# Optimization experiments

Hardware: AMD Instinct MI355X
Metric: run time of the kernel (lower is better)

The kernel has to match this reference:

```python
import jax, jax.numpy as jnp
import numpy as np

# config constants (init_kwargs)
WC, WS = 0.5, 0.5            # boundary cosine / structural weights (hybrid mode)
TARGET_BPP = 6.0             # target_bytes_per_patch
GAIN = 1.0                   # target_patch_gain
THRESH = 0.5                 # boundary_threshold; mask = p >= THRESH
EPS = 1e-6

_POP6 = jnp.array([bin(i).count('1') for i in range(64)], dtype=jnp.int32)

def _pop6(x):
    return _POP6[jnp.clip(x, 0, 63)]

def _logit(p):
    p = jnp.clip(p, EPS, 1.0 - EPS)
    return jnp.log(p) - jnp.log1p(-p)

def _next(x):  # shift-left by one, zero-padded at end (matches torch q_next pattern)
    return jnp.concatenate([x[1:], jnp.zeros((1,), x.dtype)])

def _hist(vals, mask, bins):
    idx = jnp.where(mask, vals, bins)  # invalid -> out of range, dropped
    return jnp.zeros((bins,), jnp.int32).at[idx].add(1, mode='drop')


def setup_inputs() -> dict:
    key = jax.random.key(0)
    ks = jax.random.split(key, 6)
    B, S = 4, 1048576
    return {
        'boundary_logprobs': jax.random.normal(ks[0], (B, S), jnp.float32),
        'states': jax.random.randint(ks[1], (B, S), 0, 4096, jnp.int32),
        'q_class': jax.random.randint(ks[2], (B, S), 0, 64, jnp.int32),
        'family': jax.random.randint(ks[3], (B, S), 0, 4, jnp.int32),
        'micro_ref': jax.random.randint(ks[4], (B, S), 0, 64, jnp.int32),
        'valid_mask': jax.random.randint(ks[5], (B, S), 0, 2, jnp.int32).astype(bool),
    }


def reference(boundary_logprobs, states, q_class, family, micro_ref, valid_mask):
    B, S = valid_mask.shape
    v = valid_mask.reshape(-1)
    st = states.reshape(-1).astype(jnp.int32)
    q = q_class.reshape(-1).astype(jnp.int32)
    fam = family.reshape(-1).astype(jnp.int32)
    mic = micro_ref.reshape(-1).astype(jnp.int32)

    # --- structural boundary probs ---
    omega12 = st & 0xFFF
    c6 = ((omega12 >> 6) ^ omega12) & 63          # chirality6
    d_chi = jnp.clip(_pop6(c6 ^ _next(c6)).astype(jnp.float32) / 6.0, 0.0, 1.0)
    d_q = _pop6((q & 63) ^ (_next(q) & 63)).astype(jnp.float32) / 6.0
    fx = (fam & 3) ^ (_next(fam) & 3)
    d_fam = (((fx & 1) != 0).astype(jnp.float32) + ((fx & 2) != 0).astype(jnp.float32)) / 2.0
    score = jnp.clip(0.5 * d_chi + 0.35 * d_q + 0.15 * d_fam, EPS, 1.0)
    structural = jnp.where(v, score, 0.0)

    # --- combine with cosine probs (hybrid mode) ---
    cosine = jnp.exp(jnp.minimum(boundary_logprobs.reshape(-1), 0.0))
    combined = (WC * cosine + WS * structural) / max(WC + WS, 1e-6)

    # --- target bytes-per-patch rate adjustment ---
    vf = v.astype(jnp.float32)
    vc = jnp.maximum(jnp.sum(vf), 1.0)
    cur = jnp.clip(jnp.sum(combined * vf) / vc, 1e-4, 1.0 - 1e-4)
    tgt = max(1e-4, min(1.0 - 1e-4, 1.0 / TARGET_BPP))
    shift = _logit(jnp.asarray(tgt, jnp.float32)) - _logit(cur)
    combined = jax.nn.sigmoid(_logit(combined) + GAIN * shift)
    combined = jnp.clip(combined, EPS, 1.0 - EPS)
    combined_logprobs = jnp.log(combined)
    bmask = combined_logprobs >= jnp.log(jnp.asarray(THRESH, jnp.float32))

    # --- histograms over effective (valid) positions ---
    shell = _pop6(c6)
    q_hist64 = _hist(q, v, 64)
    family_hist4 = _hist(fam, v, 4)
    micro_hist64 = _hist(mic, v, 64)
    shell_hist7 = _hist(shell, v, 7)
    wt_q = _pop6(q & 63)
    q_weight_hist7 = _hist(wt_q, v, 7)
    bits = ((q & 63)[:, None] >> jnp.arange(6)) & 1            # [n, 6]
    bit_excitation6 = jnp.sum(bits * v[:, None].astype(jnp.int32), axis=0)

    # --- patch lengths (vectorized run-length over valid bytes) ---
    bv = bmask & v
    pos = jnp.cumsum(v.astype(jnp.int32))                      # 1-indexed valid position
    bpos = jnp.where(bv, pos, 0)
    prev = jax.lax.cummax(jnp.concatenate([jnp.zeros((1,), jnp.int32), bpos[:-1]]))
    lengths = jnp.where(bv, pos - prev, 0)                     # dense run lengths at boundaries
    total_valid = pos[-1]
    trailing = total_valid - jax.lax.cummax(bpos)[-1]          # open trailing run
    patch_count = jnp.sum(bv).astype(jnp.int32) + (trailing > 0).astype(jnp.int32)

    return (combined_logprobs.reshape(B, S), bmask.reshape(B, S), structural.reshape(B, S),
            q_hist64, family_hist4, micro_hist64, shell_hist7, q_weight_hist7,
            bit_excitation6, lengths, trailing, patch_count)
```

## Files before the change

### kernel.cpp

```cpp
#include <hip/hip_runtime.h>

#define TPB 256
#define EPT 8
#define CHUNK (TPB * EPT)
#define P2T 1024
#define NSLICE 64

typedef unsigned long long ull;

__device__ __forceinline__ ull shfl_down_u64(ull x, int off) {
    unsigned lo = (unsigned)x, hi = (unsigned)(x >> 32);
    lo = __shfl_down(lo, off, 64);
    hi = __shfl_down(hi, off, 64);
    return ((ull)hi << 32) | lo;
}

__global__ __launch_bounds__(TPB, 8) void k_pass1(
    const float* __restrict__ blp, const int* __restrict__ st,
    const int* __restrict__ q, const int* __restrict__ fam,
    const int* __restrict__ mic, const int* __restrict__ vm,
    float* __restrict__ out_structural,
    int* __restrict__ blocksum_v, double* __restrict__ blocksum_c,
    int* __restrict__ ghist, int n)
{
    __shared__ int lh2[2048];
    __shared__ int slhs[11];
    __shared__ int swv[4];
    __shared__ float swc[4];

    const int tid = threadIdx.x, lane = tid & 63, wave = tid >> 6;
    const long i0 = (long)blockIdx.x * CHUNK + (long)tid * EPT;
    const bool fast = ((long)(blockIdx.x + 1) * CHUNK <= n);

    int stv[9], qv[9], fv[9], micv[8], vmv[8];
    float bpv[8];
    if (fast) {
        const int4 sa = *(const int4*)(st + i0),  sb = *(const int4*)(st + i0 + 4);
        const int4 qa = *(const int4*)(q + i0),   qb = *(const int4*)(q + i0 + 4);
        const int4 fa = *(const int4*)(fam + i0), fb = *(const int4*)(fam + i0 + 4);
        const int4 ma = *(const int4*)(mic + i0), mb = *(const int4*)(mic + i0 + 4);
        const int4 va = *(const int4*)(vm + i0),  vb = *(const int4*)(vm + i0 + 4);
        const float4 ba = *(const float4*)(blp + i0), bb = *(const float4*)(blp + i0 + 4);
        int nst = __shfl_down(sa.x, 1, 64);
        int nq  = __shfl_down(qa.x, 1, 64);
        int nf  = __shfl_down(fa.x, 1, 64);
        if (lane == 63) {
            const long j = i0 + 8;
            nst = (j < n) ? st[j]  : 0;
            nq  = (j < n) ? q[j]   : 0;
            nf  = (j < n) ? fam[j] : 0;
        }
        stv[0]=sa.x; stv[1]=sa.y; stv[2]=sa.z; stv[3]=sa.w; stv[4]=sb.x; stv[5]=sb.y; stv[6]=sb.z; stv[7]=sb.w; stv[8]=nst;
        qv[0]=qa.x;  qv[1]=qa.y;  qv[2]=qa.z;  qv[3]=qa.w;  qv[4]=qb.x;  qv[5]=qb.y;  qv[6]=qb.z;  qv[7]=qb.w;  qv[8]=nq;
        fv[0]=fa.x;  fv[1]=fa.y;  fv[2]=fa.z;  fv[3]=fa.w;  fv[4]=fb.x;  fv[5]=fb.y;  fv[6]=fb.z;  fv[7]=fb.w;  fv[8]=nf;
        micv[0]=ma.x; micv[1]=ma.y; micv[2]=ma.z; micv[3]=ma.w; micv[4]=mb.x; micv[5]=mb.y; micv[6]=mb.z; micv[7]=mb.w;
        vmv[0]=va.x; vmv[1]=va.y; vmv[2]=va.z; vmv[3]=va.w; vmv[4]=vb.x; vmv[5]=vb.y; vmv[6]=vb.z; vmv[7]=vb.w;
        bpv[0]=ba.x; bpv[1]=ba.y; bpv[2]=ba.z; bpv[3]=ba.w; bpv[4]=bb.x; bpv[5]=bb.y; bpv[6]=bb.z; bpv[7]=bb.w;
    } else {
        #pragma unroll
        for (int e = 0; e < 8; ++e) {
            long ii = i0 + e;
            bool r = ii < n;
            stv[e] = r ? st[ii] : 0;  qv[e] = r ? q[ii] : 0;  fv[e] = r ? fam[ii] : 0;
            micv[e] = r ? mic[ii] : 0; vmv[e] = r ? vm[ii] : 0; bpv[e] = r ? blp[ii] : 0.f;
        }
        stv[8] = (i0 + 8 < n) ? st[i0 + 8] : 0;
        qv[8]  = (i0 + 8 < n) ? q[i0 + 8] : 0;
        fv[8]  = (i0 + 8 < n) ? fam[i0 + 8] : 0;
    }

    {
        int4 z4; z4.x = 0; z4.y = 0; z4.z = 0; z4.w = 0;
        *(int4*)&lh2[tid * 8] = z4;
        *(int4*)&lh2[tid * 8 + 4] = z4;
    }
    if (tid < 11) slhs[tid] = 0;
    __syncthreads();

    const int qrow = ((wave << 2) | (lane & 3)) << 6;
    int sv = 0;
    float scf = 0.0f;
    ull accF = 0, accS0 = 0, accS1 = 0;
    float structural[8];
    #pragma unroll
    for (int e = 0; e < 8; ++e) {
        int sti = stv[e], qi = qv[e], fi = fv[e], mi = micv[e];
        int v = (vmv[e] != 0);
        int om  = sti & 0xFFF;      int c6  = ((om  >> 6) ^ om ) & 63;
        int omn = stv[e+1] & 0xFFF; int c6n = ((omn >> 6) ^ omn) & 63;
        float d_chi = (float)__popc(c6 ^ c6n) * (1.0f / 6.0f);
        float d_q   = (float)__popc((qi & 63) ^ (qv[e+1] & 63)) * (1.0f / 6.0f);
        int fx = (fi & 3) ^ (fv[e+1] & 3);
        float d_fam = (float)((fx & 1) + ((fx >> 1) & 1)) * 0.5f;
        float score = 0.5f * d_chi + 0.35f * d_q + 0.15f * d_fam;
        score = fminf(fmaxf(score, 1e-6f), 1.0f);
        structural[e] = v ? score : 0.0f;
        float cosine = expf(fminf(bpv[e], 0.0f));
        float combined = 0.5f * (cosine + structural[e]);
        if (v) {
            sv += 1;
            scf += combined;
            atomicAdd(&lh2[qrow + (qi & 63)], 1);
            atomicAdd(&lh2[1024 + qrow + (mi & 63)], 1);
            accF += 1ULL << ((fi & 3) * 16);
            int sh = __popc(c6);
            ull ts = 1ULL << ((sh & 3) * 16);
            if (sh < 4) accS0 += ts; else accS1 += ts;
        }
    }

    if (fast) {
        float4 o;
        o.x=structural[0]; o.y=structural[1]; o.z=structural[2]; o.w=structural[3];
        *(float4*)(out_structural + i0) = o;
        o.x=structural[4]; o.y=structural[5]; o.z=structural[6]; o.w=structural[7];
        *(float4*)(out_structural + i0 + 4) = o;
    } else {
        #pragma unroll
        for (int e = 0; e < 8; ++e)
            if (i0 + e < n) out_structural[i0 + e] = structural[e];
    }

    #pragma unroll
    for (int off = 32; off > 0; off >>= 1) {
        sv  += __shfl_down(sv, off, 64);
        scf += __shfl_down(scf, off, 64);
        accF  += shfl_down_u64(accF, off);
        accS0 += shfl_down_u64(accS0, off);
        accS1 += shfl_down_u64(accS1, off);
    }
    if (lane == 0) {
        swv[wave] = sv; swc[wave] = scf;
        #pragma unroll
        for (int b2 = 0; b2 < 4; ++b2) atomicAdd(&slhs[b2],     (int)((accF  >> (16*b2)) & 0xFFFF));
        #pragma unroll
        for (int b2 = 0; b2 < 4; ++b2) atomicAdd(&slhs[4 + b2], (int)((accS0 >> (16*b2)) & 0xFFFF));
        #pragma unroll
        for (int b2 = 0; b2 < 3; ++b2) atomicAdd(&slhs[8 + b2], (int)((accS1 >> (16*b2)) & 0xFFFF));
    }
    __syncthreads();
    if (tid == 0) {
        blocksum_v[blockIdx.x] = swv[0] + swv[1] + swv[2] + swv[3];
        blocksum_c[blockIdx.x] = (double)swc[0] + (double)swc[1] + (double)swc[2] + (double)swc[3];
    }
    int* gh = ghist + (blockIdx.x & (NSLICE - 1)) * 152;
    for (int t2 = tid; t2 < 139; t2 += TPB) {
        int val;
        if (t2 < 64) {
            val = 0;
            #pragma unroll
            for (int r = 0; r < 16; ++r) val += lh2[(r << 6) + t2];
        } else if (t2 < 68) {
            val = slhs[t2 - 64];
        } else if (t2 < 132) {
            int b2 = t2 - 68;
            val = 0;
            #pragma unroll
            for (int r = 0; r < 16; ++r) val += lh2[1024 + (r << 6) + b2];
        } else {
            val = slhs[4 + (t2 - 132)];
        }
        if (val) atomicAdd(&gh[t2], val);
    }
}

__global__ __launch_bounds__(TPB, 8) void k_pass3(
    const float* __restrict__ strc, const float* __restrict__ blp,
    const int* __restrict__ bsv, const double* __restrict__ bsc,
    const int* __restrict__ ghist,
    float* __restrict__ out_logp, float* __restrict__ out_bmask,
    float* __restrict__ out_len, int* __restrict__ chunk_cnt,
    int* __restrict__ chunk_last, ull* __restrict__ chunk_first,
    int* __restrict__ totalv_p, float* __restrict__ out_hist, int n)
{
    __shared__ int swt[4], swm[4], scnt[4];
    __shared__ ull sfirst[4];
    __shared__ int sB[4], sT[4];
    __shared__ double sC[4];
    __shared__ int qh[64];
    const int tid = threadIdx.x, lane = tid & 63, wave = tid >> 6;
    const long i0 = (long)blockIdx.x * CHUNK + (long)tid * EPT;
    const bool fast = ((long)(blockIdx.x + 1) * CHUNK <= n);
    const int nb = (int)gridDim.x;

    float sv8[8], bp8[8];
    if (fast) {
        const float4 s0 = *(const float4*)(strc + i0), s1 = *(const float4*)(strc + i0 + 4);
        const float4 p0 = *(const float4*)(blp + i0),  p1 = *(const float4*)(blp + i0 + 4);
        sv8[0]=s0.x; sv8[1]=s0.y; sv8[2]=s0.z; sv8[3]=s0.w; sv8[4]=s1.x; sv8[5]=s1.y; sv8[6]=s1.z; sv8[7]=s1.w;
        bp8[0]=p0.x; bp8[1]=p0.y; bp8[2]=p0.z; bp8[3]=p0.w; bp8[4]=p1.x; bp8[5]=p1.y; bp8[6]=p1.z; bp8[7]=p1.w;
    } else {
        #pragma unroll
        for (int e = 0; e < 8; ++e) {
            long ii = i0 + e;
            bool r = ii < n;
            sv8[e] = r ? strc[ii] : 0.0f;
            bp8[e] = r ? blp[ii] : 0.0f;
        }
    }

    int bsum = 0, tsum = 0;
    double csum = 0.0;
    for (int c = tid; c < nb; c += TPB) {
        int vv = bsv[c];
        tsum += vv;
        if (c < (int)blockIdx.x) bsum += vv;
        csum += bsc[c];
    }
    #pragma unroll
    for (int off = 32; off > 0; off >>= 1) {
        bsum += __shfl_down(bsum, off, 64);
        tsum += __shfl_down(tsum, off, 64);
        csum += __shfl_down(csum, off, 64);
    }
    if (lane == 0) { sB[wave] = bsum; sT[wave] = tsum; sC[wave] = csum; }
    __syncthreads();
    const int wb0     = sB[0] + sB[1] + sB[2] + sB[3];
    const int total_v = sT[0] + sT[1] + sT[2] + sT[3];
    const double dtot = sC[0] + sC[1] + sC[2] + sC[3];
    float shift;
    {
        double vc = (double)(total_v > 1 ? total_v : 1);
        float cur = (float)(dtot / vc);
        cur = fminf(fmaxf(cur, 1e-4f), 0.9999f);
        float p = fminf(fmaxf(cur, 1e-6f), 0.999999f);
        float lc = logf(p) - log1pf(-p);
        float tgt = (float)(1.0 / 6.0);
        float lt = logf(tgt) - log1pf(-tgt);
        shift = lt - lc;
    }

    unsigned mv = 0, mb = 0;
    float lp[8], bmf[8], lenv[8];
    #pragma unroll
    for (int e = 0; e < 8; ++e) {
        float s = sv8[e];
        int v = (s > 0.0f);
        float cosine = expf(fminf(bp8[e], 0.0f));
        float comb = 0.5f * (cosine + s);
        float p = fminf(fmaxf(comb, 1e-6f), 0.999999f);
        float z = logf(p) - log1pf(-p) + shift;
        float sgm = 1.0f / (1.0f + expf(-z));
        sgm = fminf(fmaxf(sgm, 1e-6f), 0.999999f);
        float clp = logf(sgm);
        lp[e] = clp;
        int bm = (clp >= -0.69314718f) ? 1 : 0;
        bmf[e] = (float)bm;
        mv |= (unsigned)v << e;
        if (bm & v) mb |= 1u << e;
        lenv[e] = 0.0f;
    }
    if (fast) {
        float4 o;
        o.x=lp[0]; o.y=lp[1]; o.z=lp[2]; o.w=lp[3];     *(float4*)(out_logp + i0) = o;
        o.x=lp[4]; o.y=lp[5]; o.z=lp[6]; o.w=lp[7];     *(float4*)(out_logp + i0 + 4) = o;
        o.x=bmf[0]; o.y=bmf[1]; o.z=bmf[2]; o.w=bmf[3]; *(float4*)(out_bmask + i0) = o;
        o.x=bmf[4]; o.y=bmf[5]; o.z=bmf[6]; o.w=bmf[7]; *(float4*)(out_bmask + i0 + 4) = o;
    } else {
        #pragma unroll
        for (int e = 0; e < 8; ++e)
            if (i0 + e < n) { out_logp[i0 + e] = lp[e]; out_bmask[i0 + e] = bmf[e]; }
    }

    int tvc = __popc(mv);
    int x = tvc;
    #pragma unroll
    for (int off = 1; off < 64; off <<= 1) {
        int y = __shfl_up(x, off, 64);
        if (lane >= off) x += y;
    }
    if (lane == 63) swt[wave] = x;
    __syncthreads();
    int wb = wb0;
    for (int w2 = 0; w2 < wave; ++w2) wb += swt[w2];
    const int vbase = wb + (x - tvc);

    int last = -1;
    if (mb) {
        int hb = 31 - __clz(mb);
        last = vbase + __popc(mv & ((2u << hb) - 1));
    }
    int m = last;
    #pragma unroll
    for (int off = 1; off < 64; off <<= 1) {
        int y = __shfl_up(m, off, 64);
        if (lane >= off && y > m) m = y;
    }
    int exm = __shfl_up(m, 1, 64);
    if (lane == 0) exm = -1;
    if (lane == 63) swm[wave] = m;
    int cnt = __popc(mb);
    ull fp = ~0ULL;
    if (mb) {
        int lb = __ffs(mb) - 1;
        int fv2 = vbase + __popc(mv & ((2u << lb) - 1));
        fp = ((ull)(unsigned)(i0 + lb) << 32) | (unsigned)fv2;
    }
    #pragma unroll
    for (int off = 32; off > 0; off >>= 1) {
        cnt += __shfl_down(cnt, off, 64);
        ull fo = shfl_down_u64(fp, off);
        if (fo < fp) fp = fo;
    }
    if (lane == 0) { scnt[wave] = cnt; sfirst[wave] = fp; }
    __syncthreads();

    int prev = exm;
    for (int w2 = 0; w2 < wave; ++w2) if (swm[w2] > prev) prev = swm[w2];
    int runv = 0;
    #pragma unroll
    for (int e = 0; e < 8; ++e) {
        runv += (mv >> e) & 1;
        if ((mb >> e) & 1) {
            int pos = vbase + runv;
            lenv[e] = (prev >= 0) ? (float)(pos - prev) : 0.0f;
            prev = pos;
        }
    }
    if (fast) {
        float4 o;
        o.x=lenv[0]; o.y=lenv[1]; o.z=lenv[2]; o.w=lenv[3]; *(float4*)(out_len + i0) = o;
        o.x=lenv[4]; o.y=lenv[5]; o.z=lenv[6]; o.w=lenv[7]; *(float4*)(out_len + i0 + 4) = o;
    } else {
        #pragma unroll
        for (int e = 0; e < 8; ++e)
            if (i0 + e < n) out_len[i0 + e] = lenv[e];
    }
    if (tid == 0) {
        int c = scnt[0] + scnt[1] + scnt[2] + scnt[3];
        int L = swm[0];
        if (swm[1] > L) L = swm[1];
        if (swm[2] > L) L = swm[2];
        if (swm[3] > L) L = swm[3];
        ull F = sfirst[0];
        if (sfirst[1] < F) F = sfirst[1];
        if (sfirst[2] < F) F = sfirst[2];
        if (sfirst[3] < F) F = sfirst[3];
        chunk_cnt[blockIdx.x] = c;
        chunk_last[blockIdx.x] = L > 0 ? L : 0;
        chunk_first[blockIdx.x] = F;
    }

    if (blockIdx.x == 0) {
        if (tid < 139) {
            int acc = 0;
            #pragma unroll 8
            for (int sl = 0; sl < NSLICE; ++sl) acc += ghist[sl * 152 + tid];
            out_hist[tid] = (float)acc;
            if (tid < 64) qh[tid] = acc;
        }
        if (tid == 0) *totalv_p = total_v;
        __syncthreads();
        if (tid < 7) {
            int sacc = 0;
            for (int b = 0; b < 64; ++b) if (__popc(b) == tid) sacc += qh[b];
            out_hist[139 + tid] = (float)sacc;
        }
        if (tid < 6) {
            int sacc = 0;
            for (int b = 0; b < 64; ++b) sacc += qh[b] * ((b >> tid) & 1);
            out_hist[146 + tid] = (float)sacc;
        }
    }
}

__global__ __launch_bounds__(P2T) void k_pass4(
    const int* __restrict__ chunk_cnt, const int* __restrict__ chunk_last,
    const ull* __restrict__ chunk_first, const int* __restrict__ totalv_p,
    int nb, float* __restrict__ out_len,
    float* __restrict__ out_trailing, float* __restrict__ out_patch)
{
    __shared__ int s[P2T];
    __shared__ int cs[P2T];
    int t = threadIdx.x;
    int c0 = 2 * t, c1 = 2 * t + 1;
    int a = 0, b = 0;
    if (c0 < nb) { int z = chunk_last[c0]; a = z > 0 ? z : 0; }
    if (c1 < nb) { int z = chunk_last[c1]; b = z > 0 ? z : 0; }
    int cnt = ((c0 < nb) ? chunk_cnt[c0] : 0) + ((c1 < nb) ? chunk_cnt[c1] : 0);
    s[t] = a > b ? a : b;
    cs[t] = cnt;
    __syncthreads();
    for (int off = 1; off < P2T; off <<= 1) {
        int y = (t >= off) ? s[t - off] : 0;
        __syncthreads();
        if (y > s[t]) s[t] = y;
        __syncthreads();
    }
    int excl = (t > 0) ? s[t - 1] : 0;
    int carry0 = excl;
    int carry1 = excl > a ? excl : a;
    if (c0 < nb) {
        ull F = chunk_first[c0];
        if (F != ~0ULL) {
            int fi = (int)(F >> 32);
            int fv2 = (int)(F & 0xFFFFFFFFu);
            out_len[fi] = (float)(fv2 - carry0);
        }
    }
    if (c1 < nb) {
        ull F = chunk_first[c1];
        if (F != ~0ULL) {
            int fi = (int)(F >> 32);
            int fv2 = (int)(F & 0xFFFFFFFFu);
            out_len[fi] = (float)(fv2 - carry1);
        }
    }
    int gmax = s[P2T - 1];
    __syncthreads();
    for (int off = P2T / 2; off > 0; off >>= 1) {
        if (t < off) cs[t] += cs[t + off];
        __syncthreads();
    }
    if (t == 0) {
        int total_v = *totalv_p;
        int trailing = total_v - gmax;
        int patch = cs[0] + (trailing > 0 ? 1 : 0);
        *out_trailing = (float)trailing;
        *out_patch = (float)patch;
    }
}

extern "C" void kernel_launch(void* const* d_in, const int* in_sizes, int n_in,
                              void* d_out, int out_size, void* d_ws, size_t ws_size,
                              hipStream_t stream)
{
    const float* blp = (const float*)d_in[0];
    const int* st   = (const int*)d_in[1];
    const int* q    = (const int*)d_in[2];
    const int* fam  = (const int*)d_in[3];
    const int* mic  = (const int*)d_in[4];
    const int* vm   = (const int*)d_in[5];
    const int n = in_sizes[0];
    const int nb = (n + CHUNK - 1) / CHUNK;

    float* out = (float*)d_out;
    float* out_logp       = out;
    float* out_bmask      = out + (size_t)n;
    float* out_structural = out + 2 * (size_t)n;
    float* out_hist       = out + 3 * (size_t)n;
    float* out_len        = out + 3 * (size_t)n + 152;
    float* out_trailing   = out + 4 * (size_t)n + 152;
    float* out_patch      = out + 4 * (size_t)n + 153;

    char* w = (char*)d_ws;
    int*    ghist      = (int*)(w);
    int*    blocksum_v = (int*)(w + 40960);
    int*    chunk_cnt  = (int*)(w + 73728);
    int*    chunk_last = (int*)(w + 90112);
    int*    totalv_p   = (int*)(w + 106500);
    double* blocksum_c = (double*)(w + 110592);
    ull*    chunk_first= (ull*)(w + 131072);

    hipMemsetAsync(ghist, 0, NSLICE * 152 * 4, stream);

    k_pass1<<<dim3(nb), dim3(TPB), 0, stream>>>(
        blp, st, q, fam, mic, vm, out_structural,
        blocksum_v, blocksum_c, ghist, n);

    k_pass3<<<dim3(nb), dim3(TPB), 0, stream>>>(
        out_structural, blp, blocksum_v, blocksum_c, ghist,
        out_logp, out_bmask, out_len, chunk_cnt, chunk_last, chunk_first,
        totalv_p, out_hist, n);

    k_pass4<<<dim3(1), dim3(P2T), 0, stream>>>(
        chunk_cnt, chunk_last, chunk_first, totalv_p, nb, out_len,
        out_trailing, out_patch);
}
```

Baseline: 193.1 us.

## Replace block-sum rescans with decoupled look-back scans and drop final kernel

```diff
diff --git a/kernel.cpp b/kernel.cpp
--- a/kernel.cpp
+++ b/kernel.cpp
@@ -3,10 +3,10 @@
 #define TPB 256
 #define EPT 8
 #define CHUNK (TPB * EPT)
-#define P2T 1024
 #define NSLICE 64
 
 typedef unsigned long long ull;
+typedef long long ll;
 
 __device__ __forceinline__ ull shfl_down_u64(ull x, int off) {
     unsigned lo = (unsigned)x, hi = (unsigned)(x >> 32);
@@ -15,13 +15,14 @@
     return ((ull)hi << 32) | lo;
 }
 
-__global__ __launch_bounds__(TPB, 8) void k_pass1(
+__global__ __launch_bounds__(TPB, 8) void k_passA(
     const float* __restrict__ blp, const int* __restrict__ st,
     const int* __restrict__ q, const int* __restrict__ fam,
     const int* __restrict__ mic, const int* __restrict__ vm,
     float* __restrict__ out_structural,
-    int* __restrict__ blocksum_v, double* __restrict__ blocksum_c,
-    int* __restrict__ ghist, int n)
+    int* __restrict__ ghist, ull* __restrict__ lookA,
+    int* __restrict__ pos_offset, float* __restrict__ shiftp,
+    int* __restrict__ totalv_p, int n)
 {
     __shared__ int lh2[2048];
     __shared__ int slhs[11];
@@ -139,49 +140,95 @@
         for (int b2 = 0; b2 < 3; ++b2) atomicAdd(&slhs[8 + b2], (int)((accS1 >> (16*b2)) & 0xFFFF));
     }
     __syncthreads();
-    if (tid == 0) {
-        blocksum_v[blockIdx.x] = swv[0] + swv[1] + swv[2] + swv[3];
-        blocksum_c[blockIdx.x] = (double)swc[0] + (double)swc[1] + (double)swc[2] + (double)swc[3];
-    }
-    int* gh = ghist + (blockIdx.x & (NSLICE - 1)) * 152;
-    for (int t2 = tid; t2 < 139; t2 += TPB) {
-        int val;
-        if (t2 < 64) {
-            val = 0;
+
+    if (wave != 0) {
+        int t2 = tid - 64;
+        if (t2 < 139) {
+            int val;
+            if (t2 < 64) {
+                val = 0;
+                #pragma unroll
+                for (int r = 0; r < 16; ++r) val += lh2[(r << 6) + t2];
+            } else if (t2 < 68) {
+                val = slhs[t2 - 64];
+            } else if (t2 < 132) {
+                int b2 = t2 - 68;
+                val = 0;
+                #pragma unroll
+                for (int r = 0; r < 16; ++r) val += lh2[1024 + (r << 6) + b2];
+            } else {
+                val = slhs[4 + (t2 - 132)];
+            }
+            if (val) atomicAdd(&ghist[(blockIdx.x & (NSLICE - 1)) * 152 + t2], val);
+        }
+    } else {
+        const int b = blockIdx.x;
+        const ll lv = (ll)(swv[0] + swv[1] + swv[2] + swv[3]);
+        const double lcd = (double)swc[0] + (double)swc[1] + (double)swc[2] + (double)swc[3];
+        const ll lcf = (ll)(lcd * 16384.0 + 0.5);
+        if (lane == 0)
+            atomicExch(&lookA[b], (1ULL << 62) | ((ull)lv << 39) | (ull)lcf);
+        ll exV = 0, exC = 0;
+        int base = b - 1;
+        while (base >= 0) {
+            int idx = base - lane;
+            ull w; int stt;
+            for (;;) {
+                w = (idx >= 0) ? atomicAdd(&lookA[idx], 0ULL) : (2ULL << 62);
+                stt = (int)(w >> 62);
+                if (!__ballot(stt == 0)) break;
+                __builtin_amdgcn_s_sleep(1);
+            }
+            ull incm = __ballot(stt == 2);
+            int stop = incm ? (__ffsll((ll)incm) - 1) : 64;
+            ll v = 0, c = 0;
+            if (lane <= stop && idx >= 0) {
+                v = (ll)((w >> 39) & 0x7FFFFFULL);
+                c = (ll)(w & 0x7FFFFFFFFFULL);
+            }
             #pragma unroll
-            for (int r = 0; r < 16; ++r) val += lh2[(r << 6) + t2];
-        } else if (t2 < 68) {
-            val = slhs[t2 - 64];
-        } else if (t2 < 132) {
-            int b2 = t2 - 68;
-            val = 0;
-            #pragma unroll
-            for (int r = 0; r < 16; ++r) val += lh2[1024 + (r << 6) + b2];
-        } else {
-            val = slhs[4 + (t2 - 132)];
-        }
-        if (val) atomicAdd(&gh[t2], val);
+            for (int off = 32; off > 0; off >>= 1) {
+                v += (ll)shfl_down_u64((ull)v, off);
+                c += (ll)shfl_down_u64((ull)c, off);
+            }
+            exV += v; exC += c;
+            if (stop < 64) break;
+            base -= 64;
+        }
+        if (lane == 0) {
+            atomicExch(&lookA[b], (2ULL << 62) | ((ull)(exV + lv) << 39) | (ull)(exC + lcf));
+            pos_offset[b] = (int)exV;
+            if (b == (int)gridDim.x - 1) {
+                int tv = (int)(exV + lv);
+                *totalv_p = tv;
+                double vc = (double)(tv > 1 ? tv : 1);
+                float cur = (float)(((double)(exC + lcf) * (1.0 / 16384.0)) / vc);
+                cur = fminf(fmaxf(cur, 1e-4f), 0.9999f);
+                float p = fminf(fmaxf(cur, 1e-6f), 0.999999f);
+                float lc = logf(p) - log1pf(-p);
+                float tgt = (float)(1.0 / 6.0);
+                float lt = logf(tgt) - log1pf(-tgt);
+                *shiftp = lt - lc;
+            }
+        }
     }
 }
 
-__global__ __launch_bounds__(TPB, 8) void k_pass3(
+__global__ __launch_bounds__(TPB, 8) void k_passB(
     const float* __restrict__ strc, const float* __restrict__ blp,
-    const int* __restrict__ bsv, const double* __restrict__ bsc,
-    const int* __restrict__ ghist,
+    const int* __restrict__ pos_offset, const float* __restrict__ shiftp,
+    const int* __restrict__ totalv_p, const int* __restrict__ ghist,
+    ull* __restrict__ lookB,
     float* __restrict__ out_logp, float* __restrict__ out_bmask,
-    float* __restrict__ out_len, int* __restrict__ chunk_cnt,
-    int* __restrict__ chunk_last, ull* __restrict__ chunk_first,
-    int* __restrict__ totalv_p, float* __restrict__ out_hist, int n)
+    float* __restrict__ out_len, float* __restrict__ out_hist,
+    float* __restrict__ out_trailing, float* __restrict__ out_patch, int n)
 {
     __shared__ int swt[4], swm[4], scnt[4];
-    __shared__ ull sfirst[4];
-    __shared__ int sB[4], sT[4];
-    __shared__ double sC[4];
+    __shared__ int sCarry;
     __shared__ int qh[64];
     const int tid = threadIdx.x, lane = tid & 63, wave = tid >> 6;
     const long i0 = (long)blockIdx.x * CHUNK + (long)tid * EPT;
     const bool fast = ((long)(blockIdx.x + 1) * CHUNK <= n);
-    const int nb = (int)gridDim.x;
 
     float sv8[8], bp8[8];
     if (fast) {
@@ -199,36 +246,9 @@
         }
     }
 
-    int bsum = 0, tsum = 0;
-    double csum = 0.0;
-    for (int c = tid; c < nb; c += TPB) {
-        int vv = bsv[c];
-        tsum += vv;
-        if (c < (int)blockIdx.x) bsum += vv;
-        csum += bsc[c];
-    }
-    #pragma unroll
-    for (int off = 32; off > 0; off >>= 1) {
-        bsum += __shfl_down(bsum, off, 64);
-        tsum += __shfl_down(tsum, off, 64);
-        csum += __shfl_down(csum, off, 64);
-    }
-    if (lane == 0) { sB[wave] = bsum; sT[wave] = tsum; sC[wave] = csum; }
-    __syncthreads();
-    const int wb0     = sB[0] + sB[1] + sB[2] + sB[3];
-    const int total_v = sT[0] + sT[1] + sT[2] + sT[3];
-    const double dtot = sC[0] + sC[1] + sC[2] + sC[3];
-    float shift;
-    {
-        double vc = (double)(total_v > 1 ? total_v : 1);
-        float cur = (float)(dtot / vc);
-        cur = fminf(fmaxf(cur, 1e-4f), 0.9999f);
-        float p = fminf(fmaxf(cur, 1e-6f), 0.999999f);
-        float lc = logf(p) - log1pf(-p);
-        float tgt = (float)(1.0 / 6.0);
-        float lt = logf(tgt) - log1pf(-tgt);
-        shift = lt - lc;
-    }
+    const float shift = *shiftp;
+    const int wb0 = pos_offset[blockIdx.x];
+    const float K = expf(-shift);
 
     unsigned mv = 0, mb = 0;
     float lp[8], bmf[8], lenv[8];
@@ -239,8 +259,8 @@
         float cosine = expf(fminf(bp8[e], 0.0f));
         float comb = 0.5f * (cosine + s);
         float p = fminf(fmaxf(comb, 1e-6f), 0.999999f);
-        float z = logf(p) - log1pf(-p) + shift;
-        float sgm = 1.0f / (1.0f + expf(-z));
+        float d = fmaf(K, 1.0f - p, p);
+        float sgm = p / d;
         sgm = fminf(fmaxf(sgm, 1e-6f), 0.999999f);
         float clp = logf(sgm);
         lp[e] = clp;
@@ -290,22 +310,67 @@
     if (lane == 0) exm = -1;
     if (lane == 63) swm[wave] = m;
     int cnt = __popc(mb);
-    ull fp = ~0ULL;
-    if (mb) {
-        int lb = __ffs(mb) - 1;
-        int fv2 = vbase + __popc(mv & ((2u << lb) - 1));
-        fp = ((ull)(unsigned)(i0 + lb) << 32) | (unsigned)fv2;
-    }
-    #pragma unroll
-    for (int off = 32; off > 0; off >>= 1) {
+    #pragma unroll
+    for (int off = 32; off > 0; off >>= 1)
         cnt += __shfl_down(cnt, off, 64);
-        ull fo = shfl_down_u64(fp, off);
-        if (fo < fp) fp = fo;
-    }
-    if (lane == 0) { scnt[wave] = cnt; sfirst[wave] = fp; }
+    if (lane == 0) scnt[wave] = cnt;
     __syncthreads();
 
-    int prev = exm;
+    if (wave == 0) {
+        const int b = blockIdx.x;
+        int Lown = swm[0];
+        if (swm[1] > Lown) Lown = swm[1];
+        if (swm[2] > Lown) Lown = swm[2];
+        if (swm[3] > Lown) Lown = swm[3];
+        if (Lown < 0) Lown = 0;
+        const ll Cown = (ll)(scnt[0] + scnt[1] + scnt[2] + scnt[3]);
+        if (lane == 0)
+            atomicExch(&lookB[b], (1ULL << 62) | ((ull)Lown << 23) | (ull)Cown);
+        ll exM = 0, exC = 0;
+        int base = b - 1;
+        while (base >= 0) {
+            int idx = base - lane;
+            ull w; int stt;
+            for (;;) {
+                w = (idx >= 0) ? atomicAdd(&lookB[idx], 0ULL) : (2ULL << 62);
+                stt = (int)(w >> 62);
+                if (!__ballot(stt == 0)) break;
+                __builtin_amdgcn_s_sleep(1);
+            }
+            ull incm = __ballot(stt == 2);
+            int stop = incm ? (__ffsll((ll)incm) - 1) : 64;
+            ll mm = 0, c = 0;
+            if (lane <= stop && idx >= 0) {
+                mm = (ll)((w >> 23) & 0x7FFFFFULL);
+                c  = (ll)(w & 0x7FFFFFULL);
+            }
+            #pragma unroll
+            for (int off = 32; off > 0; off >>= 1) {
+                ll mo = (ll)shfl_down_u64((ull)mm, off);
+                if (mo > mm) mm = mo;
+                c += (ll)shfl_down_u64((ull)c, off);
+            }
+            if (mm > exM) exM = mm;
+            exC += c;
+            if (stop < 64) break;
+            base -= 64;
+        }
+        if (lane == 0) {
+            ll incM = exM > (ll)Lown ? exM : (ll)Lown;
+            atomicExch(&lookB[b], (2ULL << 62) | ((ull)incM << 23) | (ull)(exC + Cown));
+            sCarry = (int)exM;
+            if (b == (int)gridDim.x - 1) {
+                int tv = *totalv_p;
+                int trailing = tv - (int)incM;
+                *out_trailing = (float)trailing;
+                *out_patch = (float)((int)(exC + Cown) + (trailing > 0 ? 1 : 0));
+            }
+        }
+    }
+    __syncthreads();
+
+    int prev = sCarry;
+    if (exm > prev) prev = exm;
     for (int w2 = 0; w2 < wave; ++w2) if (swm[w2] > prev) prev = swm[w2];
     int runv = 0;
     #pragma unroll
@@ -313,7 +378,7 @@
         runv += (mv >> e) & 1;
         if ((mb >> e) & 1) {
             int pos = vbase + runv;
-            lenv[e] = (prev >= 0) ? (float)(pos - prev) : 0.0f;
+            lenv[e] = (float)(pos - prev);
             prev = pos;
         }
     }
@@ -325,20 +390,6 @@
         #pragma unroll
         for (int e = 0; e < 8; ++e)
             if (i0 + e < n) out_len[i0 + e] = lenv[e];
-    }
-    if (tid == 0) {
-        int c = scnt[0] + scnt[1] + scnt[2] + scnt[3];
-        int L = swm[0];
-        if (swm[1] > L) L = swm[1];
-        if (swm[2] > L) L = swm[2];
-        if (swm[3] > L) L = swm[3];
-        ull F = sfirst[0];
-        if (sfirst[1] < F) F = sfirst[1];
-        if (sfirst[2] < F) F = sfirst[2];
-        if (sfirst[3] < F) F = sfirst[3];
-        chunk_cnt[blockIdx.x] = c;
-        chunk_last[blockIdx.x] = L > 0 ? L : 0;
-        chunk_first[blockIdx.x] = F;
     }
 
     if (blockIdx.x == 0) {
@@ -349,7 +400,6 @@
             out_hist[tid] = (float)acc;
             if (tid < 64) qh[tid] = acc;
         }
-        if (tid == 0) *totalv_p = total_v;
         __syncthreads();
         if (tid < 7) {
             int sacc = 0;
@@ -361,63 +411,6 @@
             for (int b = 0; b < 64; ++b) sacc += qh[b] * ((b >> tid) & 1);
             out_hist[146 + tid] = (float)sacc;
         }
-    }
-}
-
-__global__ __launch_bounds__(P2T) void k_pass4(
-    const int* __restrict__ chunk_cnt, const int* __restrict__ chunk_last,
-    const ull* __restrict__ chunk_first, const int* __restrict__ totalv_p,
-    int nb, float* __restrict__ out_len,
-    float* __restrict__ out_trailing, float* __restrict__ out_patch)
-{
-    __shared__ int s[P2T];
-    __shared__ int cs[P2T];
-    int t = threadIdx.x;
-    int c0 = 2 * t, c1 = 2 * t + 1;
-    int a = 0, b = 0;
-    if (c0 < nb) { int z = chunk_last[c0]; a = z > 0 ? z : 0; }
-    if (c1 < nb) { int z = chunk_last[c1]; b = z > 0 ? z : 0; }
-    int cnt = ((c0 < nb) ? chunk_cnt[c0] : 0) + ((c1 < nb) ? chunk_cnt[c1] : 0);
-    s[t] = a > b ? a : b;
-    cs[t] = cnt;
-    __syncthreads();
-    for (int off = 1; off < P2T; off <<= 1) {
-        int y = (t >= off) ? s[t - off] : 0;
-        __syncthreads();
-        if (y > s[t]) s[t] = y;
-        __syncthreads();
-    }
-    int excl = (t > 0) ? s[t - 1] : 0;
-    int carry0 = excl;
-    int carry1 = excl > a ? excl : a;
-    if (c0 < nb) {
-        ull F = chunk_first[c0];
-        if (F != ~0ULL) {
-            int fi = (int)(F >> 32);
-            int fv2 = (int)(F & 0xFFFFFFFFu);
-            out_len[fi] = (float)(fv2 - carry0);
-        }
-    }
-    if (c1 < nb) {
-        ull F = chunk_first[c1];
-        if (F != ~0ULL) {
-            int fi = (int)(F >> 32);
-            int fv2 = (int)(F & 0xFFFFFFFFu);
-            out_len[fi] = (float)(fv2 - carry1);
-        }
-    }
-    int gmax = s[P2T - 1];
-    __syncthreads();
-    for (int off = P2T / 2; off > 0; off >>= 1) {
-        if (t < off) cs[t] += cs[t + off];
-        __syncthreads();
-    }
-    if (t == 0) {
-        int total_v = *totalv_p;
-        int trailing = total_v - gmax;
-        int patch = cs[0] + (trailing > 0 ? 1 : 0);
-        *out_trailing = (float)trailing;
-        *out_patch = (float)patch;
     }
 }
 
@@ -445,25 +438,19 @@
 
     char* w = (char*)d_ws;
     int*    ghist      = (int*)(w);
-    int*    blocksum_v = (int*)(w + 40960);
-    int*    chunk_cnt  = (int*)(w + 73728);
-    int*    chunk_last = (int*)(w + 90112);
-    int*    totalv_p   = (int*)(w + 106500);
-    double* blocksum_c = (double*)(w + 110592);
-    ull*    chunk_first= (ull*)(w + 131072);
-
-    hipMemsetAsync(ghist, 0, NSLICE * 152 * 4, stream);
-
-    k_pass1<<<dim3(nb), dim3(TPB), 0, stream>>>(
+    ull*    lookA      = (ull*)(w + 40960);
+    ull*    lookB      = (ull*)(w + 57344);
+    int*    pos_offset = (int*)(w + 73728);
+    float*  shiftp     = (float*)(w + 81920);
+    int*    totalv_p   = (int*)(w + 81924);
+
+    hipMemsetAsync(w, 0, 73728, stream);
+
+    k_passA<<<dim3(nb), dim3(TPB), 0, stream>>>(
         blp, st, q, fam, mic, vm, out_structural,
-        blocksum_v, blocksum_c, ghist, n);
-
-    k_pass3<<<dim3(nb), dim3(TPB), 0, stream>>>(
-        out_structural, blp, blocksum_v, blocksum_c, ghist,
-        out_logp, out_bmask, out_len, chunk_cnt, chunk_last, chunk_first,
-        totalv_p, out_hist, n);
-
-    k_pass4<<<dim3(1), dim3(P2T), 0, stream>>>(
-        chunk_cnt, chunk_last, chunk_first, totalv_p, nb, out_len,
-        out_trailing, out_patch);
+        ghist, lookA, pos_offset, shiftp, totalv_p, n);
+
+    k_passB<<<dim3(nb), dim3(TPB), 0, stream>>>(
+        out_structural, blp, pos_offset, shiftp, totalv_p, ghist, lookB,
+        out_logp, out_bmask, out_len, out_hist, out_trailing, out_patch, n);
 }
```

Measured after the change: 192.9 us. About the same (-0.1%).

## Pre-reduce block sums with packed atomics, defer prefix offsets, simplify sigmoid

Applied to the files above, without the earlier changes.

```diff
diff --git a/kernel.cpp b/kernel.cpp
--- a/kernel.cpp
+++ b/kernel.cpp
@@ -7,6 +7,7 @@
 #define NSLICE 64
 
 typedef unsigned long long ull;
+typedef long long ll;
 
 __device__ __forceinline__ ull shfl_down_u64(ull x, int off) {
     unsigned lo = (unsigned)x, hi = (unsigned)(x >> 32);
@@ -20,8 +21,7 @@
     const int* __restrict__ q, const int* __restrict__ fam,
     const int* __restrict__ mic, const int* __restrict__ vm,
     float* __restrict__ out_structural,
-    int* __restrict__ blocksum_v, double* __restrict__ blocksum_c,
-    int* __restrict__ ghist, int n)
+    int* __restrict__ ghist, ull* __restrict__ l1sum, int n)
 {
     __shared__ int lh2[2048];
     __shared__ int slhs[11];
@@ -140,11 +140,13 @@
     }
     __syncthreads();
     if (tid == 0) {
-        blocksum_v[blockIdx.x] = swv[0] + swv[1] + swv[2] + swv[3];
-        blocksum_c[blockIdx.x] = (double)swc[0] + (double)swc[1] + (double)swc[2] + (double)swc[3];
-    }
-    int* gh = ghist + (blockIdx.x & (NSLICE - 1)) * 152;
-    for (int t2 = tid; t2 < 139; t2 += TPB) {
+        int vsum = swv[0] + swv[1] + swv[2] + swv[3];
+        double cs = (double)swc[0] + (double)swc[1] + (double)swc[2] + (double)swc[3];
+        ll cf = (ll)(cs * 16384.0 + 0.5);
+        atomicAdd(&l1sum[blockIdx.x >> 5], ((ull)(unsigned)vsum << 39) | (ull)cf);
+    }
+    if (tid < 139) {
+        const int t2 = tid;
         int val;
         if (t2 < 64) {
             val = 0;
@@ -160,23 +162,20 @@
         } else {
             val = slhs[4 + (t2 - 132)];
         }
-        if (val) atomicAdd(&gh[t2], val);
+        if (val) atomicAdd(&ghist[(blockIdx.x & (NSLICE - 1)) * 152 + t2], val);
     }
 }
 
 __global__ __launch_bounds__(TPB, 8) void k_pass3(
     const float* __restrict__ strc, const float* __restrict__ blp,
-    const int* __restrict__ bsv, const double* __restrict__ bsc,
-    const int* __restrict__ ghist,
+    const ull* __restrict__ l1sum, const int* __restrict__ ghist,
     float* __restrict__ out_logp, float* __restrict__ out_bmask,
     float* __restrict__ out_len, int* __restrict__ chunk_cnt,
-    int* __restrict__ chunk_last, ull* __restrict__ chunk_first,
-    int* __restrict__ totalv_p, float* __restrict__ out_hist, int n)
+    int* __restrict__ chunk_lastloc, ull* __restrict__ chunk_first,
+    int* __restrict__ chunk_vsum, float* __restrict__ out_hist, int n)
 {
     __shared__ int swt[4], swm[4], scnt[4];
-    __shared__ ull sfirst[4];
-    __shared__ int sB[4], sT[4];
-    __shared__ double sC[4];
+    __shared__ float sShift;
     __shared__ int qh[64];
     const int tid = threadIdx.x, lane = tid & 63, wave = tid >> 6;
     const long i0 = (long)blockIdx.x * CHUNK + (long)tid * EPT;
@@ -199,36 +198,32 @@
         }
     }
 
-    int bsum = 0, tsum = 0;
-    double csum = 0.0;
-    for (int c = tid; c < nb; c += TPB) {
-        int vv = bsv[c];
-        tsum += vv;
-        if (c < (int)blockIdx.x) bsum += vv;
-        csum += bsc[c];
-    }
-    #pragma unroll
-    for (int off = 32; off > 0; off >>= 1) {
-        bsum += __shfl_down(bsum, off, 64);
-        tsum += __shfl_down(tsum, off, 64);
-        csum += __shfl_down(csum, off, 64);
-    }
-    if (lane == 0) { sB[wave] = bsum; sT[wave] = tsum; sC[wave] = csum; }
-    __syncthreads();
-    const int wb0     = sB[0] + sB[1] + sB[2] + sB[3];
-    const int total_v = sT[0] + sT[1] + sT[2] + sT[3];
-    const double dtot = sC[0] + sC[1] + sC[2] + sC[3];
-    float shift;
-    {
-        double vc = (double)(total_v > 1 ? total_v : 1);
-        float cur = (float)(dtot / vc);
-        cur = fminf(fmaxf(cur, 1e-4f), 0.9999f);
-        float p = fminf(fmaxf(cur, 1e-6f), 0.999999f);
-        float lc = logf(p) - log1pf(-p);
-        float tgt = (float)(1.0 / 6.0);
-        float lt = logf(tgt) - log1pf(-tgt);
-        shift = lt - lc;
-    }
+    if (wave == 0) {
+        const int ngrp = (nb + 31) >> 5;
+        int vt = 0; ll ct = 0;
+        for (int gg = lane; gg < ngrp; gg += 64) {
+            ull cell = l1sum[gg];
+            vt += (int)(cell >> 39);
+            ct += (ll)(cell & ((1ULL << 39) - 1));
+        }
+        #pragma unroll
+        for (int off = 32; off > 0; off >>= 1) {
+            vt += __shfl_down(vt, off, 64);
+            ct += (ll)shfl_down_u64((ull)ct, off);
+        }
+        if (lane == 0) {
+            double vcd = (double)(vt > 1 ? vt : 1);
+            float cur = (float)(((double)ct * (1.0 / 16384.0)) / vcd);
+            cur = fminf(fmaxf(cur, 1e-4f), 0.9999f);
+            float p = fminf(fmaxf(cur, 1e-6f), 0.999999f);
+            float lc = logf(p) - log1pf(-p);
+            float tgt = (float)(1.0 / 6.0);
+            float lt = logf(tgt) - log1pf(-tgt);
+            sShift = lt - lc;
+        }
+    }
+    __syncthreads();
+    const float K = expf(-sShift);
 
     unsigned mv = 0, mb = 0;
     float lp[8], bmf[8], lenv[8];
@@ -239,8 +234,8 @@
         float cosine = expf(fminf(bp8[e], 0.0f));
         float comb = 0.5f * (cosine + s);
         float p = fminf(fmaxf(comb, 1e-6f), 0.999999f);
-        float z = logf(p) - log1pf(-p) + shift;
-        float sgm = 1.0f / (1.0f + expf(-z));
+        float d = fmaf(K, 1.0f - p, p);
+        float sgm = p / d;
         sgm = fminf(fmaxf(sgm, 1e-6f), 0.999999f);
         float clp = logf(sgm);
         lp[e] = clp;
@@ -271,7 +266,7 @@
     }
     if (lane == 63) swt[wave] = x;
     __syncthreads();
-    int wb = wb0;
+    int wb = 0;
     for (int w2 = 0; w2 < wave; ++w2) wb += swt[w2];
     const int vbase = wb + (x - tvc);
 
@@ -302,6 +297,7 @@
         ull fo = shfl_down_u64(fp, off);
         if (fo < fp) fp = fo;
     }
+    __shared__ ull sfirst[4];
     if (lane == 0) { scnt[wave] = cnt; sfirst[wave] = fp; }
     __syncthreads();
 
@@ -337,8 +333,9 @@
         if (sfirst[2] < F) F = sfirst[2];
         if (sfirst[3] < F) F = sfirst[3];
         chunk_cnt[blockIdx.x] = c;
-        chunk_last[blockIdx.x] = L > 0 ? L : 0;
+        chunk_lastloc[blockIdx.x] = L > 0 ? L : 0;
         chunk_first[blockIdx.x] = F;
+        chunk_vsum[blockIdx.x] = swt[0] + swt[1] + swt[2] + swt[3];
     }
 
     if (blockIdx.x == 0) {
@@ -349,7 +346,6 @@
             out_hist[tid] = (float)acc;
             if (tid < 64) qh[tid] = acc;
         }
-        if (tid == 0) *totalv_p = total_v;
         __syncthreads();
         if (tid < 7) {
             int sacc = 0;
@@ -365,59 +361,72 @@
 }
 
 __global__ __launch_bounds__(P2T) void k_pass4(
-    const int* __restrict__ chunk_cnt, const int* __restrict__ chunk_last,
-    const ull* __restrict__ chunk_first, const int* __restrict__ totalv_p,
+    const int* __restrict__ chunk_cnt, const int* __restrict__ chunk_lastloc,
+    const ull* __restrict__ chunk_first, const int* __restrict__ chunk_vsum,
     int nb, float* __restrict__ out_len,
     float* __restrict__ out_trailing, float* __restrict__ out_patch)
 {
-    __shared__ int s[P2T];
-    __shared__ int cs[P2T];
+    __shared__ int ss[P2T];
+    __shared__ int sm[P2T];
+    __shared__ int sc[P2T];
     int t = threadIdx.x;
     int c0 = 2 * t, c1 = 2 * t + 1;
-    int a = 0, b = 0;
-    if (c0 < nb) { int z = chunk_last[c0]; a = z > 0 ? z : 0; }
-    if (c1 < nb) { int z = chunk_last[c1]; b = z > 0 ? z : 0; }
-    int cnt = ((c0 < nb) ? chunk_cnt[c0] : 0) + ((c1 < nb) ? chunk_cnt[c1] : 0);
-    s[t] = a > b ? a : b;
-    cs[t] = cnt;
+    int v0 = (c0 < nb) ? chunk_vsum[c0] : 0;
+    int v1 = (c1 < nb) ? chunk_vsum[c1] : 0;
+    int l0 = (c0 < nb) ? chunk_lastloc[c0] : 0;
+    int l1 = (c1 < nb) ? chunk_lastloc[c1] : 0;
+    int k0 = (c0 < nb) ? chunk_cnt[c0] : 0;
+    int k1 = (c1 < nb) ? chunk_cnt[c1] : 0;
+    ss[t] = v0 + v1;
+    sc[t] = k0 + k1;
     __syncthreads();
     for (int off = 1; off < P2T; off <<= 1) {
-        int y = (t >= off) ? s[t - off] : 0;
-        __syncthreads();
-        if (y > s[t]) s[t] = y;
-        __syncthreads();
-    }
-    int excl = (t > 0) ? s[t - 1] : 0;
-    int carry0 = excl;
-    int carry1 = excl > a ? excl : a;
+        int add = (t >= off) ? ss[t - off] : 0;
+        __syncthreads();
+        ss[t] += add;
+        __syncthreads();
+    }
+    const int vbase0 = ss[t] - v0 - v1;
+    const int vbase1 = ss[t] - v1;
+    const int total_v = ss[P2T - 1];
+    const int gl0 = (l0 > 0) ? vbase0 + l0 : 0;
+    const int gl1 = (l1 > 0) ? vbase1 + l1 : 0;
+    sm[t] = gl0 > gl1 ? gl0 : gl1;
+    __syncthreads();
+    for (int off = 1; off < P2T; off <<= 1) {
+        int y = (t >= off) ? sm[t - off] : 0;
+        __syncthreads();
+        if (y > sm[t]) sm[t] = y;
+        __syncthreads();
+    }
+    const int excl = (t > 0) ? sm[t - 1] : 0;
     if (c0 < nb) {
         ull F = chunk_first[c0];
         if (F != ~0ULL) {
             int fi = (int)(F >> 32);
-            int fv2 = (int)(F & 0xFFFFFFFFu);
-            out_len[fi] = (float)(fv2 - carry0);
-        }
-    }
+            int fv = (int)(F & 0xFFFFFFFFu);
+            out_len[fi] = (float)(vbase0 + fv - excl);
+        }
+    }
+    const int carry1 = excl > gl0 ? excl : gl0;
     if (c1 < nb) {
         ull F = chunk_first[c1];
         if (F != ~0ULL) {
             int fi = (int)(F >> 32);
-            int fv2 = (int)(F & 0xFFFFFFFFu);
-            out_len[fi] = (float)(fv2 - carry1);
-        }
-    }
-    int gmax = s[P2T - 1];
+            int fv = (int)(F & 0xFFFFFFFFu);
+            out_len[fi] = (float)(vbase1 + fv - carry1);
+        }
+    }
+    const int gmax = sm[P2T - 1];
     __syncthreads();
     for (int off = P2T / 2; off > 0; off >>= 1) {
-        if (t < off) cs[t] += cs[t + off];
+        if (t < off) sc[t] += sc[t + off];
         __syncthreads();
     }
     if (t == 0) {
-        int total_v = *totalv_p;
         int trailing = total_v - gmax;
-        int patch = cs[0] + (trailing > 0 ? 1 : 0);
         *out_trailing = (float)trailing;
-        *out_patch = (float)patch;
+        *out_patch = (float)(sc[0] + (trailing > 0 ? 1 : 0));
     }
 }
 
@@ -444,26 +453,24 @@
     float* out_patch      = out + 4 * (size_t)n + 153;
 
     char* w = (char*)d_ws;
-    int*    ghist      = (int*)(w);
-    int*    blocksum_v = (int*)(w + 40960);
-    int*    chunk_cnt  = (int*)(w + 73728);
-    int*    chunk_last = (int*)(w + 90112);
-    int*    totalv_p   = (int*)(w + 106500);
-    double* blocksum_c = (double*)(w + 110592);
-    ull*    chunk_first= (ull*)(w + 131072);
-
-    hipMemsetAsync(ghist, 0, NSLICE * 152 * 4, stream);
+    int*  ghist         = (int*)(w);
+    ull*  l1sum         = (ull*)(w + 38912);
+    int*  chunk_cnt     = (int*)(w + 40960);
+    int*  chunk_lastloc = (int*)(w + 49152);
+    int*  chunk_vsum    = (int*)(w + 57344);
+    ull*  chunk_first   = (ull*)(w + 65536);
+
+    hipMemsetAsync(w, 0, 39424, stream);
 
     k_pass1<<<dim3(nb), dim3(TPB), 0, stream>>>(
-        blp, st, q, fam, mic, vm, out_structural,
-        blocksum_v, blocksum_c, ghist, n);
+        blp, st, q, fam, mic, vm, out_structural, ghist, l1sum, n);
 
     k_pass3<<<dim3(nb), dim3(TPB), 0, stream>>>(
-        out_structural, blp, blocksum_v, blocksum_c, ghist,
-        out_logp, out_bmask, out_len, chunk_cnt, chunk_last, chunk_first,
-        totalv_p, out_hist, n);
+        out_structural, blp, l1sum, ghist,
+        out_logp, out_bmask, out_len, chunk_cnt, chunk_lastloc, chunk_first,
+        chunk_vsum, out_hist, n);
 
     k_pass4<<<dim3(1), dim3(P2T), 0, stream>>>(
-        chunk_cnt, chunk_last, chunk_first, totalv_p, nb, out_len,
+        chunk_cnt, chunk_lastloc, chunk_first, chunk_vsum, nb, out_len,
         out_trailing, out_patch);
 }
```

New measurement: 173.4 us. 10.2% less time.
